# Performance work log

Measured on AMD Instinct MI355X. Metric: run time of the kernel, lower is better.

The kernel has to match this reference:

```python
import jax, jax.numpy as jnp
import numpy as np

B, H, L, D, S = 32, 1, 4096, 64, 512  # batch, heads(=1, codebook shared), seq, d_k, n_code
PE_LAM = 100000.0
EPS = 1e-6


def _sinusoid_embs(length, width, lam):
    # standard sinusoid table [length, width]: concat(sin, cos)
    pos = jnp.arange(length, dtype=jnp.float32)
    inv_lams = lam ** (-jnp.arange(0, width, 2, dtype=jnp.float32) / width)
    pre = pos[:, None] * inv_lams[None, :]
    return jnp.concatenate([jnp.sin(pre), jnp.cos(pre)], axis=-1)


def _codebook():
    # get_codebook: sinusoids -> rms-norm (center/gain/bias off) -> tau^{-1/2} scale -> stop-grad -> [1,S,D]
    c = _sinusoid_embs(S, D, PE_LAM)
    c = c * jax.lax.rsqrt(jnp.mean(jnp.square(c), axis=-1, keepdims=True) + EPS)
    tau = float(D) ** 0.5
    return jax.lax.stop_gradient((tau ** -0.5) * c)[None, ...]  # [H=1, S, D]


def setup_inputs() -> dict:
    key = jax.random.key(0)
    vecs = jax.random.normal(key, (B, H, L, D), dtype=jnp.float32)
    loss_mask = jnp.ones((B, L), dtype=jnp.float32)
    return {"vecs": vecs, "loss_mask": loss_mask}


def reference(vecs, loss_mask):
    c = _codebook()  # [1, S, D]
    # pairwise squared distances [B,H,L,S] via ||v||^2 - 2 v.c + ||c||^2
    diffs2 = (
        jnp.sum(jnp.square(vecs), axis=-1)[..., None]
        - 2.0 * jnp.einsum("bhlk,hsk->bhls", vecs, c)
        + jnp.sum(jnp.square(c), axis=-1)[None, :, None, :]
    )
    z = jnp.argmin(diffs2, axis=-1).astype(jnp.int32)       # [B,H,L]
    errs2 = jax.nn.relu(jnp.min(diffs2, axis=-1))           # [B,H,L]
    # gather codewords: codebook [1,1,S,D], indices [B,H,L,1]
    cz = jnp.take_along_axis(c[None, ...], z[..., None], axis=2)  # [B,H,L,D]
    # straight-through estimator
    quantized = jax.lax.stop_gradient(cz) + vecs - jax.lax.stop_gradient(vecs)
    # l_commit = mean over (B,L) of sum over heads of masked errs2
    l_commit = jnp.mean(jnp.sum(loss_mask[:, None, :] * errs2, axis=1))
    return quantized, z, l_commit, errs2
```

## Files before the change

kernel.cpp:

```cpp
#include <hip/hip_runtime.h>
#include <math.h>

#define NB 32
#define NL 4096
#define ND 64
#define NS 512
#define NTOK (NB*NL)

#define OFF_Q 0
#define OFF_Z (NTOK*ND)
#define OFF_LC (OFF_Z + NTOK)
#define OFF_E (OFF_LC + 1)

typedef __attribute__((ext_vector_type(8))) short short8;
typedef __attribute__((ext_vector_type(4))) float f32x4;
typedef unsigned int u32;
typedef unsigned short u16;
typedef unsigned long long u64;

#define QCODES 128
#define TOKS 128
#define TPB 512
#define SLOTS 12
#define SLOTP 13
#define EPS_H 1e-3f
#define NBLK (NTOK / TOKS)

__device__ __forceinline__ u32 f2bf_rne(float x) {
    u32 u = __float_as_uint(x);
    return (u + 0x7fffu + ((u >> 16) & 1u)) >> 16;
}

__device__ __forceinline__ void upd_key(u64& best, float dist, int code) {
    u32 u = __float_as_uint(dist);
    u ^= (u >> 31) ? 0xFFFFFFFFu : 0x80000000u;
    u64 k = ((u64)u << 32) | (u32)code;
    if (k < best) best = k;
}

__global__ void cb_kernel(float* __restrict__ cb, float* __restrict__ cc,
                          u16* __restrict__ cbh, u16* __restrict__ cbl) {
    int s = blockIdx.x;
    int d = threadIdx.x;
    int j = (d < 32) ? d : (d - 32);
    double e = -(double)(2 * j) / 64.0;
    double invlam = pow(100000.0, e);
    double pre = (double)s * invlam;
    float val = (float)((d < 32) ? sin(pre) : cos(pre));

    float sq = val * val;
    #pragma unroll
    for (int off = 32; off > 0; off >>= 1) sq += __shfl_xor(sq, off);
    float mean = sq * (1.0f / 64.0f);
    float scale = (1.0f / sqrtf(mean + 1e-6f)) * 0.35355339059327379f;
    float c = val * scale;
    cb[s * ND + d] = c;

    float c2 = c * c;
    #pragma unroll
    for (int off = 32; off > 0; off >>= 1) c2 += __shfl_xor(c2, off);
    if (d == 0) cc[s] = c2;

    u32 hb = f2bf_rne(c);
    float hf = __uint_as_float(hb << 16);
    u32 lb = f2bf_rne(c - hf);
    int g = d >> 3, ee = d & 7;
    int pos = s * 64 + (((g ^ (s & 7)) << 3) | ee);
    cbh[pos] = (u16)hb;
    cbl[pos] = (u16)lb;
}

__launch_bounds__(TPB, 3)
__global__ void fused_kernel(const float* __restrict__ vecs,
                             const float* __restrict__ mask,
                             const float* __restrict__ cb,
                             const float* __restrict__ cc,
                             const u16* __restrict__ cbh,
                             const u16* __restrict__ cbl,
                             float* __restrict__ outq,
                             float* __restrict__ outz,
                             float* __restrict__ oute,
                             float* __restrict__ partial) {
    __shared__ u16 ldsH[QCODES * 64];
    __shared__ u16 ldsL[QCODES * 64];
    __shared__ u32 slots[TOKS * SLOTP];
    __shared__ float hval[TOKS * SLOTP];
    __shared__ u32 cnt_l[TOKS];
    __shared__ int z_l[TOKS];
    __shared__ float wsum[TPB / 64];

    const int tid = threadIdx.x;
    const int grp = blockIdx.x;
    const int w = tid >> 6;
    const int lane = tid & 63;
    const int c16 = lane & 15;
    const int h = lane >> 4;

    #pragma unroll
    for (int i = 0; i < 2; ++i) {
        int k = i * TPB + tid;
        ((short8*)ldsH)[k] = ((const short8*)cbh)[k];
        ((short8*)ldsL)[k] = ((const short8*)cbl)[k];
    }
    if (tid < TOKS) cnt_l[tid] = 0;

    const int trow = w * 16 + c16;
    short8 bh[2], bl[2];
    {
        const float* vp = vecs + (size_t)(grp * TOKS + trow) * ND;
        #pragma unroll
        for (int kk = 0; kk < 2; ++kk) {
            const float4* pp = (const float4*)(vp + kk * 32 + h * 8);
            float4 t0 = pp[0], t1 = pp[1];
            float x[8] = {t0.x, t0.y, t0.z, t0.w, t1.x, t1.y, t1.z, t1.w};
            short8 H, L;
            #pragma unroll
            for (int e2 = 0; e2 < 8; ++e2) {
                u32 hb = f2bf_rne(x[e2]);
                float hf = __uint_as_float(hb << 16);
                u32 lb = f2bf_rne(x[e2] - hf);
                H[e2] = (short)hb; L[e2] = (short)lb;
            }
            bh[kk] = H; bl[kk] = L;
        }
    }
    __syncthreads();

    for (int q = 0; q < 4; ++q) {
        short8 gh[2], gl[2];
        if (q < 3) {
            const short8* sH = (const short8*)(cbh + (q + 1) * QCODES * 64);
            const short8* sL = (const short8*)(cbl + (q + 1) * QCODES * 64);
            #pragma unroll
            for (int i = 0; i < 2; ++i) {
                gh[i] = sH[i * TPB + tid];
                gl[i] = sL[i * TPB + tid];
            }
        }

        #pragma unroll
        for (int c = 0; c < 2; ++c) {
            f32x4 acc[4];
            #pragma unroll
            for (int mt = 0; mt < 4; ++mt) {
                int cr = q * QCODES + c * 64 + mt * 16 + h * 4;
                f32x4 ini;
                ini[0] = -0.5f * cc[cr + 0];
                ini[1] = -0.5f * cc[cr + 1];
                ini[2] = -0.5f * cc[cr + 2];
                ini[3] = -0.5f * cc[cr + 3];
                acc[mt] = ini;
            }
            #pragma unroll
            for (int mt = 0; mt < 4; ++mt) {
                int code_l = c * 64 + mt * 16 + c16;
                int sw = code_l & 7;
                short8 ah[2], al[2];
                #pragma unroll
                for (int kk = 0; kk < 2; ++kk) {
                    int off = code_l * 64 + (((kk * 4 + h) ^ sw) << 3);
                    ah[kk] = *(const short8*)(ldsH + off);
                    al[kk] = *(const short8*)(ldsL + off);
                }
                #pragma unroll
                for (int kk = 0; kk < 2; ++kk) {
                    acc[mt] = __builtin_amdgcn_mfma_f32_16x16x32_bf16(ah[kk], bh[kk], acc[mt], 0, 0, 0);
                    acc[mt] = __builtin_amdgcn_mfma_f32_16x16x32_bf16(ah[kk], bl[kk], acc[mt], 0, 0, 0);
                    acc[mt] = __builtin_amdgcn_mfma_f32_16x16x32_bf16(al[kk], bh[kk], acc[mt], 0, 0, 0);
                }
            }
            float m = acc[0][0];
            #pragma unroll
            for (int mt = 0; mt < 4; ++mt) {
                m = fmaxf(m, fmaxf(fmaxf(acc[mt][0], acc[mt][1]),
                                   fmaxf(acc[mt][2], acc[mt][3])));
            }
            m = fmaxf(m, __shfl_xor(m, 16));
            m = fmaxf(m, __shfl_xor(m, 32));
            float thr = m - EPS_H;
            #pragma unroll
            for (int mt = 0; mt < 4; ++mt) {
                #pragma unroll
                for (int r = 0; r < 4; ++r) {
                    float v = acc[mt][r];
                    if (v >= thr) {
                        u32 pos = atomicAdd(&cnt_l[trow], 1u);
                        if (pos < (u32)SLOTS) {
                            slots[trow * SLOTP + pos] = (u32)(q * QCODES + c * 64 + mt * 16 + h * 4 + r);
                            hval[trow * SLOTP + pos] = v;
                        }
                    }
                }
            }
        }

        if (q < 3) {
            __syncthreads();
            #pragma unroll
            for (int i = 0; i < 2; ++i) {
                int k = i * TPB + tid;
                ((short8*)ldsH)[k] = gh[i];
                ((short8*)ldsL)[k] = gl[i];
            }
            __syncthreads();
        }
    }

    const int p  = tid >> 2;
    const int qs = tid & 3;
    const int tok = grp * TOKS + p;

    float4 vf[16];
    {
        const float4* vr = (const float4*)(vecs + (size_t)tok * ND);
        #pragma unroll
        for (int g = 0; g < 16; ++g) vf[g] = vr[g];
    }
    float vv;
    {
        float a0 = 0.f, a1 = 0.f, a2 = 0.f, a3 = 0.f;
        #pragma unroll
        for (int i = 0; i < 16; ++i) {
            a0 = fmaf(vf[i].x, vf[i].x, a0);
            a1 = fmaf(vf[i].y, vf[i].y, a1);
            a2 = fmaf(vf[i].z, vf[i].z, a2);
            a3 = fmaf(vf[i].w, vf[i].w, a3);
        }
        vv = (a0 + a1) + (a2 + a3);
    }

    u32 cnt = cnt_l[p]; if (cnt > (u32)SLOTS) cnt = (u32)SLOTS;
    float hm = -3.4e38f;
    for (u32 j2 = 0; j2 < cnt; ++j2) hm = fmaxf(hm, hval[p * SLOTP + j2]);
    float thr2 = hm - EPS_H;

    u64 best = 0xFFFFFFFFFFFFFFFFull;
    for (u32 j2 = qs; j2 < cnt; j2 += 4) {
        if (hval[p * SLOTP + j2] >= thr2) {
            int code = (int)slots[p * SLOTP + j2];
            const float4* cs = (const float4*)(cb + (size_t)code * ND);
            float d0 = 0.f, d1 = 0.f, d2 = 0.f, d3 = 0.f;
            #pragma unroll
            for (int i2 = 0; i2 < 16; ++i2) {
                float4 cv = cs[i2];
                d0 = fmaf(cv.x, vf[i2].x, d0);
                d1 = fmaf(cv.y, vf[i2].y, d1);
                d2 = fmaf(cv.z, vf[i2].z, d2);
                d3 = fmaf(cv.w, vf[i2].w, d3);
            }
            float dot = (d0 + d1) + (d2 + d3);
            float dist = (vv - 2.0f * dot) + cc[code];
            upd_key(best, dist, code);
        }
    }
    {
        u64 o = __shfl_xor(best, 1); if (o < best) best = o;
        o = __shfl_xor(best, 2); if (o < best) best = o;
    }

    float contrib = 0.0f;
    if (qs == 0) {
        int zi = (int)(best & 0xFFFFFFFFu);
        u32 du = (u32)(best >> 32);
        du ^= (du >> 31) ? 0x80000000u : 0xFFFFFFFFu;
        float dmin = __uint_as_float(du);
        float err = fmaxf(dmin, 0.0f);
        outz[tok] = (float)zi;
        oute[tok] = err;
        z_l[p] = zi;
        contrib = mask[tok] * err;
    }
    #pragma unroll
    for (int off = 32; off > 0; off >>= 1) contrib += __shfl_xor(contrib, off);
    if (lane == 0) wsum[w] = contrib;
    __syncthreads();
    if (tid == 0) {
        float t = 0.f;
        #pragma unroll
        for (int i = 0; i < TPB / 64; ++i) t += wsum[i];
        partial[grp] = t;
    }

    const float4* cb4 = (const float4*)cb;
    float4* qo = (float4*)(outq + (size_t)grp * TOKS * ND);
    #pragma unroll
    for (int i = 0; i < 4; ++i) {
        int gidx = i * TPB + tid;
        int t2 = gidx >> 4;
        int sub = gidx & 15;
        qo[gidx] = cb4[(size_t)z_l[t2] * 16 + sub];
    }
}

__global__ void fin_kernel(const float* __restrict__ partial, float* __restrict__ outl) {
    int t = threadIdx.x;
    float x = partial[t];
    #pragma unroll
    for (int off = 32; off > 0; off >>= 1) x += __shfl_xor(x, off);
    __shared__ float ws[16];
    if ((t & 63) == 0) ws[t >> 6] = x;
    __syncthreads();
    if (t == 0) {
        float s = 0.f;
        #pragma unroll
        for (int i = 0; i < 16; ++i) s += ws[i];
        outl[0] = s / (float)NTOK;
    }
}

extern "C" void kernel_launch(void* const* d_in, const int* in_sizes, int n_in,
                              void* d_out, int out_size, void* d_ws, size_t ws_size,
                              hipStream_t stream) {
    const float* vecs = (const float*)d_in[0];
    const float* mask = (const float*)d_in[1];

    float* out = (float*)d_out;
    float* outq = out + OFF_Q;
    float* outz = out + OFF_Z;
    float* outl = out + OFF_LC;
    float* oute = out + OFF_E;

    float* ws_f = (float*)d_ws;
    float* cb = ws_f;
    float* cc = ws_f + 32768;
    u16*  cbh = (u16*)(ws_f + 33280);
    u16*  cbl = (u16*)(ws_f + 49664);
    float* partial = ws_f + 66048;

    cb_kernel<<<NS, 64, 0, stream>>>(cb, cc, cbh, cbl);
    fused_kernel<<<NBLK, TPB, 0, stream>>>(vecs, mask, cb, cc, cbh, cbl,
                                           outq, outz, oute, partial);
    fin_kernel<<<1, 1024, 0, stream>>>(partial, outl);
}
```

Measured before the change: 65.94 us.

## Shrink candidate slots to u16, drop hval filter, add overflow fallback

Candidate slots are now stored as 16-bit code indices and the per-candidate approximate score array is removed, so the second-pass max/threshold filtering is gone and every recorded candidate is rescored exactly in fp32. When a token overflows its slot capacity, that token falls back to an exhaustive scan of all 512 codes, which also makes overflow handling correct rather than truncated. The smaller LDS footprint allows raising the launch-bounds occupancy target from 3 to 4 blocks per CU. The cost is more exact rescoring work per token, possibly extra register pressure, and a slow path for any overflowing tokens.

```diff
diff --git a/kernel.cpp b/kernel.cpp
--- a/kernel.cpp
+++ b/kernel.cpp
@@ -70,7 +70,7 @@
     cbl[pos] = (u16)lb;
 }
 
-__launch_bounds__(TPB, 3)
+__launch_bounds__(TPB, 4)
 __global__ void fused_kernel(const float* __restrict__ vecs,
                              const float* __restrict__ mask,
                              const float* __restrict__ cb,
@@ -83,8 +83,7 @@
                              float* __restrict__ partial) {
     __shared__ u16 ldsH[QCODES * 64];
     __shared__ u16 ldsL[QCODES * 64];
-    __shared__ u32 slots[TOKS * SLOTP];
-    __shared__ float hval[TOKS * SLOTP];
+    __shared__ u16 slots[TOKS * SLOTP];
     __shared__ u32 cnt_l[TOKS];
     __shared__ int z_l[TOKS];
     __shared__ float wsum[TPB / 64];
@@ -185,10 +184,8 @@
                     float v = acc[mt][r];
                     if (v >= thr) {
                         u32 pos = atomicAdd(&cnt_l[trow], 1u);
-                        if (pos < (u32)SLOTS) {
-                            slots[trow * SLOTP + pos] = (u32)(q * QCODES + c * 64 + mt * 16 + h * 4 + r);
-                            hval[trow * SLOTP + pos] = v;
-                        }
+                        if (pos < (u32)SLOTS)
+                            slots[trow * SLOTP + pos] = (u16)(q * QCODES + c * 64 + mt * 16 + h * 4 + r);
                     }
                 }
             }
@@ -229,14 +226,26 @@
         vv = (a0 + a1) + (a2 + a3);
     }
 
-    u32 cnt = cnt_l[p]; if (cnt > (u32)SLOTS) cnt = (u32)SLOTS;
-    float hm = -3.4e38f;
-    for (u32 j2 = 0; j2 < cnt; ++j2) hm = fmaxf(hm, hval[p * SLOTP + j2]);
-    float thr2 = hm - EPS_H;
-
     u64 best = 0xFFFFFFFFFFFFFFFFull;
-    for (u32 j2 = qs; j2 < cnt; j2 += 4) {
-        if (hval[p * SLOTP + j2] >= thr2) {
+    u32 cntraw = cnt_l[p];
+    if (cntraw > (u32)SLOTS) {
+        for (int code = qs; code < NS; code += 4) {
+            const float4* cs = (const float4*)(cb + (size_t)code * ND);
+            float d0 = 0.f, d1 = 0.f, d2 = 0.f, d3 = 0.f;
+            #pragma unroll
+            for (int i2 = 0; i2 < 16; ++i2) {
+                float4 cv = cs[i2];
+                d0 = fmaf(cv.x, vf[i2].x, d0);
+                d1 = fmaf(cv.y, vf[i2].y, d1);
+                d2 = fmaf(cv.z, vf[i2].z, d2);
+                d3 = fmaf(cv.w, vf[i2].w, d3);
+            }
+            float dot = (d0 + d1) + (d2 + d3);
+            float dist = (vv - 2.0f * dot) + cc[code];
+            upd_key(best, dist, code);
+        }
+    } else {
+        for (u32 j2 = qs; j2 < cntraw; j2 += 4) {
             int code = (int)slots[p * SLOTP + j2];
             const float4* cs = (const float4*)(cb + (size_t)code * ND);
             float d0 = 0.f, d1 = 0.f, d2 = 0.f, d3 = 0.f;
```

Result: slower. 84.95 us (+28.8%).
